# Performance work log

Measured on AMD Instinct MI355X. Metric: run time of the kernel, lower is better.

Reference implementation:

```python
import jax, jax.numpy as jnp
import numpy as np

N_OBS = 2_097_152
N_BAND = 4
T_SPAN = 3650.0  # days


def setup_inputs() -> dict:
    key = jax.random.key(0)
    k0, k1, k2, k3, k4, k5 = jax.random.split(key, 6)
    t = jnp.sort(jax.random.uniform(k0, (N_OBS,), jnp.float32) * T_SPAN)
    band = jax.random.randint(k1, (N_OBS,), 0, N_BAND)
    y = jax.random.normal(k2, (N_OBS,), jnp.float32)
    yerr = 0.1 + 0.9 * jax.random.uniform(k3, (N_OBS,), jnp.float32)
    log_amp_delta = 0.1 * jax.random.normal(k4, (N_BAND - 1,), jnp.float32)
    # [log sigma, log ell] for the quasisep Exp kernel
    log_kernel_param = jnp.array([0.0, np.log(50.0)], dtype=jnp.float32) + \
        0.1 * jax.random.normal(k5, (2,), jnp.float32)
    return {"t": t, "band": band, "y": y, "yerr": yerr,
            "log_amp_delta": log_amp_delta, "log_kernel_param": log_kernel_param}


def _log_prob(t, band, y, yerr, log_amp_delta, log_kernel_param):
    # amp_transform: prepend 0 -> per-band amplitudes
    amps = jnp.exp(jnp.concatenate([jnp.zeros(1, log_amp_delta.dtype), log_amp_delta]))
    sigma2 = jnp.exp(2.0 * log_kernel_param[0])
    ell = jnp.exp(log_kernel_param[1])

    # lag_transform with zero lags: sort by time (assume_sorted path of tinygp)
    inds = jnp.argsort(t)
    ts, b = t[inds], band[inds]
    ys, dg = y[inds], (yerr ** 2)[inds]

    # multiband Exp kernel: K_ij = sigma2 * u_i * u_j * exp(-(t_i - t_j)/ell), i>=j
    u = amps[b]                       # per-point amplitude
    a = dg + sigma2 * u * u           # diagonal K_ii + noise
    U = sigma2 * u                    # semiseparable left factor
    V = u                             # semiseparable right factor
    dt = jnp.diff(ts)
    P = jnp.concatenate([jnp.zeros(1, ts.dtype), jnp.exp(-dt / ell)])  # decay factors

    # Celerite O(N) Cholesky (K = L D L^T) fused with the forward solve L z = y.
    def step(carry, x):
        cS, cg = carry                # cS = S_{n-1} + D_{n-1} W_{n-1}^2 ; cg = g_{n-1} + W_{n-1} z_{n-1}
        Pn, an, Un, Vn, yn = x
        Sn = Pn * Pn * cS
        gn = Pn * cg
        Dn = an - Un * Un * Sn
        Wn = (Vn - Sn * Un) / Dn
        zn = yn - Un * gn
        return (Sn + Dn * Wn * Wn, gn + Wn * zn), (jnp.log(Dn), zn * zn / Dn)

    zero = jnp.zeros((), ts.dtype)
    _, (logD, quad) = jax.lax.scan(step, (zero, zero), (P, a, U, V, ys))
    n = ts.shape[0]
    return -0.5 * (jnp.sum(quad) + jnp.sum(logD) + n * jnp.log(2.0 * jnp.pi))


def reference(t, band, y, yerr, log_amp_delta, log_kernel_param):
    return _log_prob(t, band, y, yerr, log_amp_delta, log_kernel_param)
```

## Files before the change

### kernel.cpp

```cpp
#include <hip/hip_runtime.h>
#include <math.h>

#define N_TOTAL 2097152
#define NT 256
#define NC 16
#define EPB (NT * NC)
#define NB (N_TOTAL / EPB)

struct DMat { double al, be, ga, de, c, e, f; };

__device__ __forceinline__ DMat dmat_identity() {
    DMat m; m.al = 1.0; m.be = 0.0; m.ga = 0.0; m.de = 1.0; m.c = 1.0; m.e = 0.0; m.f = 0.0;
    return m;
}

__device__ __forceinline__ DMat dmat_compose(const DMat& A, const DMat& B) {
    DMat r;
    r.al = A.al * B.al + A.be * B.ga;
    r.be = A.al * B.be + A.be * B.de;
    r.ga = A.ga * B.al + A.de * B.ga;
    r.de = A.ga * B.be + A.de * B.de;
    r.c  = A.c * B.c;
    r.e  = A.e * B.al + A.c * B.e + A.f * B.ga;
    r.f  = A.e * B.be + A.c * B.f + A.f * B.de;
    return r;
}

__device__ __forceinline__ void dmat_normalize(DMat& m) {
    double mx = fmax(fabs(m.al), fabs(m.be));
    mx = fmax(mx, fabs(m.ga));
    mx = fmax(mx, fabs(m.de));
    mx = fmax(mx, fabs(m.c));
    mx = fmax(mx, fabs(m.e));
    mx = fmax(mx, fabs(m.f));
    if (!(mx > 0.0) || isinf(mx)) return;
    double inv = 1.0 / mx;
    m.al *= inv; m.be *= inv; m.ga *= inv; m.de *= inv;
    m.c *= inv; m.e *= inv; m.f *= inv;
}

__device__ __forceinline__ void dmat_store(double* sm, int i, const DMat& m) {
    sm[0 * NT + i] = m.al; sm[1 * NT + i] = m.be; sm[2 * NT + i] = m.ga;
    sm[3 * NT + i] = m.de; sm[4 * NT + i] = m.c;  sm[5 * NT + i] = m.e;
    sm[6 * NT + i] = m.f;
}

__device__ __forceinline__ DMat dmat_load(const double* sm, int i) {
    DMat m;
    m.al = sm[0 * NT + i]; m.be = sm[1 * NT + i]; m.ga = sm[2 * NT + i];
    m.de = sm[3 * NT + i]; m.c  = sm[4 * NT + i]; m.e  = sm[5 * NT + i];
    m.f  = sm[6 * NT + i];
    return m;
}

__device__ __forceinline__ DMat dmat_scan_inclusive(double* sm, DMat mine, int tid) {
    dmat_store(sm, tid, mine);
    __syncthreads();
    for (int d = 1; d < NT; d <<= 1) {
        DMat o;
        bool has = (tid >= d);
        if (has) o = dmat_load(sm, tid - d);
        __syncthreads();
        if (has) {
            mine = dmat_compose(mine, o);
            dmat_normalize(mine);
            dmat_store(sm, tid, mine);
        }
        __syncthreads();
    }
    return mine;
}

__device__ __forceinline__ DMat elem_mat_f32(float P, float dg, float s2u2,
                                             float sigma2, float u, float yy) {
    float p = P * P;
    float U = sigma2 * u;
    DMat m;
    m.al = (double)(p * (dg - s2u2));
    m.be = (double)(u * u);
    m.ga = -(double)(p * U * U);
    m.de = (double)(dg + s2u2);
    m.c  = (double)(P * dg);
    m.e  = -(double)(yy * p * U);
    m.f  = (double)(yy * u);
    return m;
}

__global__ __launch_bounds__(NT) void k_upsweep(
    const float* __restrict__ t, const int* __restrict__ band,
    const float* __restrict__ y, const float* __restrict__ yerr,
    const float* __restrict__ lad, const float* __restrict__ lkp,
    double* __restrict__ block_comp)
{
    __shared__ double sm[7 * NT];
    const int tid = threadIdx.x;
    const float sigma2 = __expf(2.f * lkp[0]);
    const float inv_ell = __expf(-lkp[1]);
    float amps[4];
    amps[0] = 1.f;
    amps[1] = __expf(lad[0]);
    amps[2] = __expf(lad[1]);
    amps[3] = __expf(lad[2]);

    const int base = (blockIdx.x * NT + tid) * NC;
    float tprev = (base == 0) ? 0.f : t[base - 1];
    DMat acc = dmat_identity();
    #pragma unroll
    for (int k = 0; k < NC; k += 4) {
        float4 tv = *reinterpret_cast<const float4*>(t + base + k);
        float4 yv = *reinterpret_cast<const float4*>(y + base + k);
        float4 ev = *reinterpret_cast<const float4*>(yerr + base + k);
        int4   bv = *reinterpret_cast<const int4*>(band + base + k);
        float tc[4] = {tv.x, tv.y, tv.z, tv.w};
        float yc[4] = {yv.x, yv.y, yv.z, yv.w};
        float ec[4] = {ev.x, ev.y, ev.z, ev.w};
        int   bc[4] = {bv.x, bv.y, bv.z, bv.w};
        #pragma unroll
        for (int j = 0; j < 4; ++j) {
            float u = amps[bc[j] & 3];
            float dg = ec[j] * ec[j];
            float s2u2 = sigma2 * u * u;
            float P = ((base + k + j) == 0) ? 0.f
                    : __expf(-(tc[j] - tprev) * inv_ell);
            acc = dmat_compose(elem_mat_f32(P, dg, s2u2, sigma2, u, yc[j]), acc);
            tprev = tc[j];
        }
    }
    dmat_normalize(acc);
    DMat incl = dmat_scan_inclusive(sm, acc, tid);
    if (tid == NT - 1) {
        double* o = block_comp + blockIdx.x * 7;
        o[0] = incl.al; o[1] = incl.be; o[2] = incl.ga; o[3] = incl.de;
        o[4] = incl.c;  o[5] = incl.e;  o[6] = incl.f;
    }
}

__global__ __launch_bounds__(NT) void k_spine(
    const double* __restrict__ block_comp, double* __restrict__ block_excl,
    double* __restrict__ accum, unsigned int* __restrict__ counter)
{
    __shared__ double sm[7 * NT];
    const int tid = threadIdx.x;
    if (tid == 0) {
        accum[0] = 0.0;
        accum[1] = 0.0;
        *counter = 0u;
    }
    const double* p0 = block_comp + (2 * tid) * 7;
    const double* p1 = block_comp + (2 * tid + 1) * 7;
    DMat m0 = {p0[0], p0[1], p0[2], p0[3], p0[4], p0[5], p0[6]};
    DMat m1 = {p1[0], p1[1], p1[2], p1[3], p1[4], p1[5], p1[6]};
    DMat mine = dmat_compose(m1, m0);
    dmat_normalize(mine);
    dmat_scan_inclusive(sm, mine, tid);
    DMat E = (tid == 0) ? dmat_identity() : dmat_load(sm, tid - 1);
    double* o0 = block_excl + (2 * tid) * 7;
    o0[0] = E.al; o0[1] = E.be; o0[2] = E.ga; o0[3] = E.de;
    o0[4] = E.c;  o0[5] = E.e;  o0[6] = E.f;
    DMat M = dmat_compose(m0, E);
    dmat_normalize(M);
    double* o1 = block_excl + (2 * tid + 1) * 7;
    o1[0] = M.al; o1[1] = M.be; o1[2] = M.ga; o1[3] = M.de;
    o1[4] = M.c;  o1[5] = M.e;  o1[6] = M.f;
}

__global__ __launch_bounds__(NT) void k_replay(
    const float* __restrict__ t, const int* __restrict__ band,
    const float* __restrict__ y, const float* __restrict__ yerr,
    const float* __restrict__ lad, const float* __restrict__ lkp,
    const double* __restrict__ block_excl, double* __restrict__ accum,
    unsigned int* __restrict__ counter, float* __restrict__ out)
{
    __shared__ double sm[7 * NT];
    const int tid = threadIdx.x;
    const float sigma2 = __expf(2.f * lkp[0]);
    const float inv_ell = __expf(-lkp[1]);
    float amps[4];
    amps[0] = 1.f;
    amps[1] = __expf(lad[0]);
    amps[2] = __expf(lad[1]);
    amps[3] = __expf(lad[2]);

    const int base = (blockIdx.x * NT + tid) * NC;
    float tprev = (base == 0) ? 0.f : t[base - 1];

    float Pv[NC], dgv[NC], uv[NC], yv_[NC];
    DMat acc = dmat_identity();
    #pragma unroll
    for (int k = 0; k < NC; k += 4) {
        float4 tv = *reinterpret_cast<const float4*>(t + base + k);
        float4 yv = *reinterpret_cast<const float4*>(y + base + k);
        float4 ev = *reinterpret_cast<const float4*>(yerr + base + k);
        int4   bv = *reinterpret_cast<const int4*>(band + base + k);
        float tc[4] = {tv.x, tv.y, tv.z, tv.w};
        float yc[4] = {yv.x, yv.y, yv.z, yv.w};
        float ec[4] = {ev.x, ev.y, ev.z, ev.w};
        int   bc[4] = {bv.x, bv.y, bv.z, bv.w};
        #pragma unroll
        for (int j = 0; j < 4; ++j) {
            float u = amps[bc[j] & 3];
            float dg = ec[j] * ec[j];
            float s2u2 = sigma2 * u * u;
            float P = ((base + k + j) == 0) ? 0.f
                    : __expf(-(tc[j] - tprev) * inv_ell);
            Pv[k + j] = P; dgv[k + j] = dg; uv[k + j] = u; yv_[k + j] = yc[j];
            acc = dmat_compose(elem_mat_f32(P, dg, s2u2, sigma2, u, yc[j]), acc);
            tprev = tc[j];
        }
    }
    dmat_normalize(acc);
    dmat_scan_inclusive(sm, acc, tid);
    DMat E = (tid == 0) ? dmat_identity() : dmat_load(sm, tid - 1);

    const double* pb = block_excl + blockIdx.x * 7;
    DMat Eb = {pb[0], pb[1], pb[2], pb[3], pb[4], pb[5], pb[6]};
    DMat F = dmat_compose(E, Eb);
    float x = 0.f, g = 0.f;
    if (F.de != 0.0) {
        double invde = 1.0 / F.de;
        x = (float)(F.be * invde);
        g = (float)(F.f  * invde);
    }
    if (!isfinite(x)) x = 0.f;
    if (!isfinite(g)) g = 0.f;

    float s_logD = 0.f, s_quad = 0.f;
    #pragma unroll
    for (int k = 0; k < NC; ++k) {
        float P = Pv[k], dg = dgv[k], u = uv[k], yy = yv_[k];
        float U = sigma2 * u;
        float a = dg + U * u;
        float p = P * P;
        float S = p * x;
        float D = a - U * U * S;
        if (!(D > 1e-30f)) D = 1e-30f;
        float W = (u - S * U) / D;
        float gn = P * g;
        float z = yy - U * gn;
        s_logD += __logf(D);
        s_quad += z * z / D;
        x = S + D * W * W;
        g = gn + W * z;
    }

    __syncthreads();
    sm[tid] = (double)s_logD;
    sm[NT + tid] = (double)s_quad;
    __syncthreads();
    for (int d = NT / 2; d > 0; d >>= 1) {
        if (tid < d) {
            sm[tid] += sm[tid + d];
            sm[NT + tid] += sm[NT + tid + d];
        }
        __syncthreads();
    }
    if (tid == 0) {
        atomicAdd(&accum[0], sm[0]);
        atomicAdd(&accum[1], sm[NT]);
        __threadfence();
        unsigned int old = atomicAdd(counter, 1u);
        if (old == NB - 1) {
            double s0 = atomicAdd(&accum[0], 0.0);
            double s1 = atomicAdd(&accum[1], 0.0);
            double r = -0.5 * (s0 + s1
                       + (double)N_TOTAL * 1.8378770664093454836);
            out[0] = (float)r;
        }
    }
}

extern "C" void kernel_launch(void* const* d_in, const int* in_sizes, int n_in,
                              void* d_out, int out_size, void* d_ws, size_t ws_size,
                              hipStream_t stream)
{
    const float* t    = (const float*)d_in[0];
    const int*   band = (const int*)d_in[1];
    const float* y    = (const float*)d_in[2];
    const float* yerr = (const float*)d_in[3];
    const float* lad  = (const float*)d_in[4];
    const float* lkp  = (const float*)d_in[5];

    double* dws        = (double*)d_ws;
    double* block_comp = dws;
    double* block_excl = dws + NB * 7;
    double* accum      = dws + 2 * NB * 7;
    unsigned int* counter = (unsigned int*)(accum + 2);

    k_upsweep<<<NB, NT, 0, stream>>>(t, band, y, yerr, lad, lkp, block_comp);
    k_spine<<<1, NT, 0, stream>>>(block_comp, block_excl, accum, counter);
    k_replay<<<NB, NT, 0, stream>>>(t, band, y, yerr, lad, lkp, block_excl,
                                    accum, counter, (float*)d_out);
}
```

Before: 126.5 us.

## Replace shared-memory block scans with wave-shuffle scans and halve per-thread chunk

Block-level prefix scans of the 7-double transfer matrices now run as 64-lane wavefront shuffle scans, with the per-wave results combined by one thread and stored to a new wave_excl buffer. This replaces eight barrier-separated shared-memory rounds. The per-thread chunk drops from 16 to 8 elements, which doubles the block count to 1024. The spine kernel therefore handles four blocks per thread, and the final reduction uses wave shuffles. The upsweep and replay kernels gain a launch-bounds occupancy hint, at the cost of an extra global buffer and serial per-wave composition.

```diff
diff --git a/kernel.cpp b/kernel.cpp
--- a/kernel.cpp
+++ b/kernel.cpp
@@ -3,9 +3,10 @@
 
 #define N_TOTAL 2097152
 #define NT 256
-#define NC 16
+#define NC 8
 #define EPB (NT * NC)
 #define NB (N_TOTAL / EPB)
+#define NWAVES (NT / 64)
 
 struct DMat { double al, be, ga, de, c, e, f; };
 
@@ -39,34 +40,26 @@
     m.c *= inv; m.e *= inv; m.f *= inv;
 }
 
-__device__ __forceinline__ void dmat_store(double* sm, int i, const DMat& m) {
-    sm[0 * NT + i] = m.al; sm[1 * NT + i] = m.be; sm[2 * NT + i] = m.ga;
-    sm[3 * NT + i] = m.de; sm[4 * NT + i] = m.c;  sm[5 * NT + i] = m.e;
-    sm[6 * NT + i] = m.f;
-}
-
-__device__ __forceinline__ DMat dmat_load(const double* sm, int i) {
-    DMat m;
-    m.al = sm[0 * NT + i]; m.be = sm[1 * NT + i]; m.ga = sm[2 * NT + i];
-    m.de = sm[3 * NT + i]; m.c  = sm[4 * NT + i]; m.e  = sm[5 * NT + i];
-    m.f  = sm[6 * NT + i];
-    return m;
-}
-
-__device__ __forceinline__ DMat dmat_scan_inclusive(double* sm, DMat mine, int tid) {
-    dmat_store(sm, tid, mine);
-    __syncthreads();
-    for (int d = 1; d < NT; d <<= 1) {
-        DMat o;
-        bool has = (tid >= d);
-        if (has) o = dmat_load(sm, tid - d);
-        __syncthreads();
-        if (has) {
+__device__ __forceinline__ DMat dmat_shfl_up(const DMat& m, int d) {
+    DMat r;
+    r.al = __shfl_up(m.al, d, 64);
+    r.be = __shfl_up(m.be, d, 64);
+    r.ga = __shfl_up(m.ga, d, 64);
+    r.de = __shfl_up(m.de, d, 64);
+    r.c  = __shfl_up(m.c,  d, 64);
+    r.e  = __shfl_up(m.e,  d, 64);
+    r.f  = __shfl_up(m.f,  d, 64);
+    return r;
+}
+
+__device__ __forceinline__ DMat dmat_wave_scan(DMat mine, int lane) {
+    #pragma unroll
+    for (int d = 1; d < 64; d <<= 1) {
+        DMat o = dmat_shfl_up(mine, d);
+        if (lane >= d) {
             mine = dmat_compose(mine, o);
             dmat_normalize(mine);
-            dmat_store(sm, tid, mine);
-        }
-        __syncthreads();
+        }
     }
     return mine;
 }
@@ -86,21 +79,29 @@
     return m;
 }
 
-__global__ __launch_bounds__(NT) void k_upsweep(
+__device__ __forceinline__ void dmat_store_g(double* p, const DMat& m) {
+    p[0] = m.al; p[1] = m.be; p[2] = m.ga; p[3] = m.de;
+    p[4] = m.c;  p[5] = m.e;  p[6] = m.f;
+}
+
+__device__ __forceinline__ DMat dmat_load_g(const double* p) {
+    DMat m = {p[0], p[1], p[2], p[3], p[4], p[5], p[6]};
+    return m;
+}
+
+__global__ __launch_bounds__(NT, 4) void k_upsweep(
     const float* __restrict__ t, const int* __restrict__ band,
     const float* __restrict__ y, const float* __restrict__ yerr,
     const float* __restrict__ lad, const float* __restrict__ lkp,
-    double* __restrict__ block_comp)
+    double* __restrict__ block_comp, double* __restrict__ wave_excl)
 {
-    __shared__ double sm[7 * NT];
+    __shared__ double smw[7 * NWAVES];
     const int tid = threadIdx.x;
+    const int lane = tid & 63;
+    const int wv = tid >> 6;
     const float sigma2 = __expf(2.f * lkp[0]);
     const float inv_ell = __expf(-lkp[1]);
-    float amps[4];
-    amps[0] = 1.f;
-    amps[1] = __expf(lad[0]);
-    amps[2] = __expf(lad[1]);
-    amps[3] = __expf(lad[2]);
+    float amps[4] = {1.f, __expf(lad[0]), __expf(lad[1]), __expf(lad[2])};
 
     const int base = (blockIdx.x * NT + tid) * NC;
     float tprev = (base == 0) ? 0.f : t[base - 1];
@@ -127,11 +128,26 @@
         }
     }
     dmat_normalize(acc);
-    DMat incl = dmat_scan_inclusive(sm, acc, tid);
-    if (tid == NT - 1) {
-        double* o = block_comp + blockIdx.x * 7;
-        o[0] = incl.al; o[1] = incl.be; o[2] = incl.ga; o[3] = incl.de;
-        o[4] = incl.c;  o[5] = incl.e;  o[6] = incl.f;
+    DMat incl = dmat_wave_scan(acc, lane);
+    if (lane == 63) {
+        #define STW(idx, val) smw[(idx) * NWAVES + wv] = (val)
+        STW(0, incl.al); STW(1, incl.be); STW(2, incl.ga); STW(3, incl.de);
+        STW(4, incl.c);  STW(5, incl.e);  STW(6, incl.f);
+        #undef STW
+    }
+    __syncthreads();
+    if (tid == 0) {
+        DMat pre = dmat_identity();
+        for (int w = 0; w < NWAVES; ++w) {
+            dmat_store_g(wave_excl + (blockIdx.x * NWAVES + w) * 7, pre);
+            DMat Ww = {smw[0 * NWAVES + w], smw[1 * NWAVES + w],
+                       smw[2 * NWAVES + w], smw[3 * NWAVES + w],
+                       smw[4 * NWAVES + w], smw[5 * NWAVES + w],
+                       smw[6 * NWAVES + w]};
+            pre = dmat_compose(Ww, pre);
+            dmat_normalize(pre);
+        }
+        dmat_store_g(block_comp + blockIdx.x * 7, pre);
     }
 }
 
@@ -139,47 +155,67 @@
     const double* __restrict__ block_comp, double* __restrict__ block_excl,
     double* __restrict__ accum, unsigned int* __restrict__ counter)
 {
-    __shared__ double sm[7 * NT];
+    __shared__ double smw[7 * NWAVES];
     const int tid = threadIdx.x;
+    const int lane = tid & 63;
+    const int wv = tid >> 6;
     if (tid == 0) {
         accum[0] = 0.0;
         accum[1] = 0.0;
         *counter = 0u;
     }
-    const double* p0 = block_comp + (2 * tid) * 7;
-    const double* p1 = block_comp + (2 * tid + 1) * 7;
-    DMat m0 = {p0[0], p0[1], p0[2], p0[3], p0[4], p0[5], p0[6]};
-    DMat m1 = {p1[0], p1[1], p1[2], p1[3], p1[4], p1[5], p1[6]};
-    DMat mine = dmat_compose(m1, m0);
-    dmat_normalize(mine);
-    dmat_scan_inclusive(sm, mine, tid);
-    DMat E = (tid == 0) ? dmat_identity() : dmat_load(sm, tid - 1);
-    double* o0 = block_excl + (2 * tid) * 7;
-    o0[0] = E.al; o0[1] = E.be; o0[2] = E.ga; o0[3] = E.de;
-    o0[4] = E.c;  o0[5] = E.e;  o0[6] = E.f;
-    DMat M = dmat_compose(m0, E);
-    dmat_normalize(M);
-    double* o1 = block_excl + (2 * tid + 1) * 7;
-    o1[0] = M.al; o1[1] = M.be; o1[2] = M.ga; o1[3] = M.de;
-    o1[4] = M.c;  o1[5] = M.e;  o1[6] = M.f;
-}
-
-__global__ __launch_bounds__(NT) void k_replay(
+    DMat m[4];
+    #pragma unroll
+    for (int i = 0; i < 4; ++i)
+        m[i] = dmat_load_g(block_comp + (4 * tid + i) * 7);
+    DMat acc = m[0];
+    #pragma unroll
+    for (int i = 1; i < 4; ++i) acc = dmat_compose(m[i], acc);
+    dmat_normalize(acc);
+    DMat incl = dmat_wave_scan(acc, lane);
+    if (lane == 63) {
+        #define STW(idx, val) smw[(idx) * NWAVES + wv] = (val)
+        STW(0, incl.al); STW(1, incl.be); STW(2, incl.ga); STW(3, incl.de);
+        STW(4, incl.c);  STW(5, incl.e);  STW(6, incl.f);
+        #undef STW
+    }
+    __syncthreads();
+    DMat wpre = dmat_identity();
+    for (int w = 0; w < wv; ++w) {
+        DMat Ww = {smw[0 * NWAVES + w], smw[1 * NWAVES + w],
+                   smw[2 * NWAVES + w], smw[3 * NWAVES + w],
+                   smw[4 * NWAVES + w], smw[5 * NWAVES + w],
+                   smw[6 * NWAVES + w]};
+        wpre = dmat_compose(Ww, wpre);
+    }
+    dmat_normalize(wpre);
+    DMat lex = dmat_shfl_up(incl, 1);
+    if (lane == 0) lex = dmat_identity();
+    DMat tex = dmat_compose(lex, wpre);
+    dmat_normalize(tex);
+    #pragma unroll
+    for (int i = 0; i < 4; ++i) {
+        dmat_store_g(block_excl + (4 * tid + i) * 7, tex);
+        tex = dmat_compose(m[i], tex);
+        dmat_normalize(tex);
+    }
+}
+
+__global__ __launch_bounds__(NT, 4) void k_replay(
     const float* __restrict__ t, const int* __restrict__ band,
     const float* __restrict__ y, const float* __restrict__ yerr,
     const float* __restrict__ lad, const float* __restrict__ lkp,
-    const double* __restrict__ block_excl, double* __restrict__ accum,
-    unsigned int* __restrict__ counter, float* __restrict__ out)
+    const double* __restrict__ block_excl, const double* __restrict__ wave_excl,
+    double* __restrict__ accum, unsigned int* __restrict__ counter,
+    float* __restrict__ out)
 {
-    __shared__ double sm[7 * NT];
+    __shared__ double smr[2 * NWAVES];
     const int tid = threadIdx.x;
+    const int lane = tid & 63;
+    const int wv = tid >> 6;
     const float sigma2 = __expf(2.f * lkp[0]);
     const float inv_ell = __expf(-lkp[1]);
-    float amps[4];
-    amps[0] = 1.f;
-    amps[1] = __expf(lad[0]);
-    amps[2] = __expf(lad[1]);
-    amps[3] = __expf(lad[2]);
+    float amps[4] = {1.f, __expf(lad[0]), __expf(lad[1]), __expf(lad[2])};
 
     const int base = (blockIdx.x * NT + tid) * NC;
     float tprev = (base == 0) ? 0.f : t[base - 1];
@@ -209,12 +245,15 @@
         }
     }
     dmat_normalize(acc);
-    dmat_scan_inclusive(sm, acc, tid);
-    DMat E = (tid == 0) ? dmat_identity() : dmat_load(sm, tid - 1);
-
-    const double* pb = block_excl + blockIdx.x * 7;
-    DMat Eb = {pb[0], pb[1], pb[2], pb[3], pb[4], pb[5], pb[6]};
-    DMat F = dmat_compose(E, Eb);
+    DMat incl = dmat_wave_scan(acc, lane);
+    DMat lex = dmat_shfl_up(incl, 1);
+    if (lane == 0) lex = dmat_identity();
+
+    DMat Ew = dmat_load_g(wave_excl + (blockIdx.x * NWAVES + wv) * 7);
+    DMat Eb = dmat_load_g(block_excl + blockIdx.x * 7);
+    DMat Fw = dmat_compose(Ew, Eb);
+    dmat_normalize(Fw);
+    DMat F = dmat_compose(lex, Fw);
     float x = 0.f, g = 0.f;
     if (F.de != 0.0) {
         double invde = 1.0 / F.de;
@@ -243,20 +282,19 @@
         g = gn + W * z;
     }
 
+    double sl = (double)s_logD, sq = (double)s_quad;
+    #pragma unroll
+    for (int d = 32; d > 0; d >>= 1) {
+        sl += __shfl_down(sl, d, 64);
+        sq += __shfl_down(sq, d, 64);
+    }
+    if (lane == 0) { smr[wv] = sl; smr[NWAVES + wv] = sq; }
     __syncthreads();
-    sm[tid] = (double)s_logD;
-    sm[NT + tid] = (double)s_quad;
-    __syncthreads();
-    for (int d = NT / 2; d > 0; d >>= 1) {
-        if (tid < d) {
-            sm[tid] += sm[tid + d];
-            sm[NT + tid] += sm[NT + tid + d];
-        }
-        __syncthreads();
-    }
     if (tid == 0) {
-        atomicAdd(&accum[0], sm[0]);
-        atomicAdd(&accum[1], sm[NT]);
+        double tl = smr[0] + smr[1] + smr[2] + smr[3];
+        double tq = smr[NWAVES] + smr[NWAVES + 1] + smr[NWAVES + 2] + smr[NWAVES + 3];
+        atomicAdd(&accum[0], tl);
+        atomicAdd(&accum[1], tq);
         __threadfence();
         unsigned int old = atomicAdd(counter, 1u);
         if (old == NB - 1) {
@@ -282,12 +320,15 @@
 
     double* dws        = (double*)d_ws;
     double* block_comp = dws;
-    double* block_excl = dws + NB * 7;
-    double* accum      = dws + 2 * NB * 7;
+    double* block_excl = block_comp + NB * 7;
+    double* wave_excl  = block_excl + NB * 7;
+    double* accum      = wave_excl + NB * NWAVES * 7;
     unsigned int* counter = (unsigned int*)(accum + 2);
 
-    k_upsweep<<<NB, NT, 0, stream>>>(t, band, y, yerr, lad, lkp, block_comp);
+    k_upsweep<<<NB, NT, 0, stream>>>(t, band, y, yerr, lad, lkp,
+                                     block_comp, wave_excl);
     k_spine<<<1, NT, 0, stream>>>(block_comp, block_excl, accum, counter);
-    k_replay<<<NB, NT, 0, stream>>>(t, band, y, yerr, lad, lkp, block_excl,
-                                    accum, counter, (float*)d_out);
-}
+    k_replay<<<NB, NT, 0, stream>>>(t, band, y, yerr, lad, lkp,
+                                    block_excl, wave_excl, accum, counter,
+                                    (float*)d_out);
+}
```

Result: slower. 138.9 us (+9.8%).
